# Performance work log

Measured on AMD Instinct MI355X. Metric: run time of the kernel, lower is better.

Reference implementation:

```python
import jax, jax.numpy as jnp
import numpy as np

HIDDEN = 128
IN = 28
SEQ = 28
OUT = 10
B = 16384


def _uniform(key, shape, k):
    return jax.random.uniform(key, shape, jnp.float32, -k, k)


def setup_inputs() -> dict:
    key = jax.random.key(0)
    ks = jax.random.split(key, 12)
    k = 1.0 / np.sqrt(HIDDEN)
    return {
        "x": jax.random.normal(ks[0], (B, SEQ * IN), jnp.float32),
        "w_ih_l0": _uniform(ks[1], (4 * HIDDEN, IN), k),
        "w_hh_l0": _uniform(ks[2], (4 * HIDDEN, HIDDEN), k),
        "b_ih_l0": _uniform(ks[3], (4 * HIDDEN,), k),
        "b_hh_l0": _uniform(ks[4], (4 * HIDDEN,), k),
        "w_ih_l1": _uniform(ks[5], (4 * HIDDEN, HIDDEN), k),
        "w_hh_l1": _uniform(ks[6], (4 * HIDDEN, HIDDEN), k),
        "b_ih_l1": _uniform(ks[7], (4 * HIDDEN,), k),
        "b_hh_l1": _uniform(ks[8], (4 * HIDDEN,), k),
        "fc_w": _uniform(ks[9], (OUT, HIDDEN), k),
        "fc_b": _uniform(ks[10], (OUT,), k),
    }


def _lstm_layer(x, w_ih, w_hh, b_ih, b_hh):
    # x: [B, T, D_in] -> hs: [B, T, H], hT/cT: [B, H]
    Bz = x.shape[0]
    H = w_hh.shape[1]
    # precompute input projection for all timesteps (one big GEMM)
    xp = jnp.einsum('btd,gd->btg', x, w_ih) + b_ih  # [B, T, 4H]
    xp = jnp.swapaxes(xp, 0, 1)  # [T, B, 4H]
    h0 = jnp.zeros((Bz, H), x.dtype)
    c0 = jnp.zeros((Bz, H), x.dtype)

    def step(carry, xt):
        h, c = carry
        gates = xt + h @ w_hh.T + b_hh  # [B, 4H]
        i, f, g, o = jnp.split(gates, 4, axis=-1)  # torch gate order i,f,g,o
        c_new = jax.nn.sigmoid(f) * c + jax.nn.sigmoid(i) * jnp.tanh(g)
        h_new = jax.nn.sigmoid(o) * jnp.tanh(c_new)
        return (h_new, c_new), h_new

    (hT, cT), hs = jax.lax.scan(step, (h0, c0), xp)
    return jnp.swapaxes(hs, 0, 1), hT, cT


def reference(x, w_ih_l0, w_hh_l0, b_ih_l0, b_hh_l0,
              w_ih_l1, w_hh_l1, b_ih_l1, b_hh_l1, fc_w, fc_b):
    x = x.reshape(-1, SEQ, IN)
    out0, h0T, c0T = _lstm_layer(x, w_ih_l0, w_hh_l0, b_ih_l0, b_hh_l0)
    out1, h1T, c1T = _lstm_layer(out0, w_ih_l1, w_hh_l1, b_ih_l1, b_hh_l1)
    logits = out1[:, -1, :] @ fc_w.T + fc_b  # [B, out_dim]
    h_n = jnp.stack([h0T, h1T], axis=0)  # [2, B, H]
    c_n = jnp.stack([c0T, c1T], axis=0)
    return (logits, h_n, c_n)
```

## Files before the change

kernel.cpp:

```cpp
#include <hip/hip_runtime.h>

typedef __attribute__((ext_vector_type(8))) short short8;
typedef __attribute__((ext_vector_type(4))) float f32x4;
typedef __attribute__((ext_vector_type(4))) unsigned int u32x4;

#define MFMA16(a, b, c) __builtin_amdgcn_mfma_f32_16x16x32_bf16((a), (b), (c), 0, 0, 0)

__device__ __forceinline__ unsigned short f2bf(float f) {
  unsigned int u = __builtin_bit_cast(unsigned int, f);
  u += 0x7fffu + ((u >> 16) & 1u);
  return (unsigned short)(u >> 16);
}
__device__ __forceinline__ float bf2f(unsigned short s) {
  unsigned int u = ((unsigned int)s) << 16;
  return __builtin_bit_cast(float, u);
}
__device__ __forceinline__ unsigned cvtpk(float lo, float hi) {
  unsigned r;
  asm("v_cvt_pk_bf16_f32 %0, %1, %2" : "=v"(r) : "v"(lo), "v"(hi));
  return r;
}

__device__ __forceinline__ void lstm_elem(float gi, float gf, float gg, float go,
                                          float& c, float& h) {
  const float L1 = 1.44269504f, L2 = 2.88539008f;
  float A = __builtin_amdgcn_exp2f(-L1 * gi);
  float B = __builtin_amdgcn_exp2f(L2 * gg);
  float t1 = 1.0f + B;
  float den = __builtin_amdgcn_rcpf(__builtin_fmaf(A, t1, t1));
  float it = (B - 1.0f) * den;
  float F = __builtin_amdgcn_rcpf(1.0f + __builtin_amdgcn_exp2f(-L1 * gf));
  c = __builtin_fmaf(F, c, it);
  float C = __builtin_amdgcn_exp2f(L2 * c);
  float O = __builtin_amdgcn_exp2f(-L1 * go);
  float t2 = 1.0f + C;
  float den2 = __builtin_amdgcn_rcpf(__builtin_fmaf(O, t2, t2));
  h = (C - 1.0f) * den2;
}

__global__ void prep_weights(const float* __restrict__ w_ih_l0, const float* __restrict__ w_hh_l0,
                             const float* __restrict__ w_ih_l1, const float* __restrict__ w_hh_l1,
                             unsigned short* __restrict__ W0f, unsigned short* __restrict__ W1f) {
  int tid = blockIdx.x * blockDim.x + threadIdx.x;
  if (tid < 32 * 5 * 64) {
    int nt = tid / 320, rem = tid % 320;
    int kc = rem / 64, lane = rem % 64;
    int g = nt * 16 + (lane & 15);
    int k0 = kc * 32 + (lane >> 4) * 8;
    short8 s;
#pragma unroll
    for (int j = 0; j < 8; ++j) {
      int k = k0 + j;
      float val;
      if (k < 28) val = w_ih_l0[g * 28 + k];
      else if (k < 32) val = 0.0f;
      else val = w_hh_l0[g * 128 + (k - 32)];
      s[j] = (short)f2bf(val);
    }
    *(short8*)(W0f + (size_t)tid * 8) = s;
  } else if (tid < 32 * 5 * 64 + 32 * 8 * 64) {
    int id = tid - 32 * 5 * 64;
    int nt = id / 512, rem = id % 512;
    int kc = rem / 64, lane = rem % 64;
    int g = nt * 16 + (lane & 15);
    int k0 = kc * 32 + (lane >> 4) * 8;
    short8 s;
#pragma unroll
    for (int j = 0; j < 8; ++j) {
      int k = k0 + j;
      float val = (k < 128) ? w_ih_l1[g * 128 + k] : w_hh_l1[g * 128 + (k - 128)];
      s[j] = (short)f2bf(val);
    }
    *(short8*)(W1f + (size_t)id * 8) = s;
  }
}

__global__ __launch_bounds__(512) void lstm_fused(
    const float* __restrict__ x,
    const float* __restrict__ b_ih_l0, const float* __restrict__ b_hh_l0,
    const float* __restrict__ b_ih_l1, const float* __restrict__ b_hh_l1,
    const float* __restrict__ fc_w, const float* __restrict__ fc_b,
    const unsigned short* __restrict__ W0f, const unsigned short* __restrict__ W1f,
    float* __restrict__ out) {
  __shared__ __align__(16) char hls[4 * 16384];

  const int tid = (int)threadIdx.x;
  const int wv = tid >> 6;
  const int lane = tid & 63;
  const int lr = lane & 15;
  const int lq = lane >> 4;
  const int b0 = (int)blockIdx.x * 64;

  for (int i = tid; i < 16384; i += 512) ((unsigned*)hls)[i] = 0u;

  f32x4 bias0s[4], bias1s[4];
#pragma unroll
  for (int q = 0; q < 4; ++q) {
    int g = q * 128 + wv * 16 + lr;
    float v0 = b_ih_l0[g] + b_hh_l0[g];
    float v1 = b_ih_l1[g] + b_hh_l1[g];
    f32x4 s0; s0[0] = v0; s0[1] = v0; s0[2] = v0; s0[3] = v0;
    f32x4 s1; s1[0] = v1; s1[1] = v1; s1[2] = v1; s1[3] = v1;
    bias0s[q] = s0; bias1s[q] = s1;
  }

  const unsigned rbB = (unsigned)(lr * 256 + ((lq ^ lr) << 4));
  const unsigned cwl = (unsigned)((wv * 2 + (lr >> 3)) ^ (lq << 2));
  const unsigned wbB = (unsigned)(lq * 1024 + (cwl << 4) + (lr & 7) * 2);
  const unsigned wB0 = (unsigned)((wv * 320 + lane) * 16);
  const unsigned wB1 = (unsigned)((wv * 512 + lane) * 16);
  const unsigned xo0 = (unsigned)(((b0 + lr) * 784 + lq * 8) * 4);

  float c0s[4][4], c1s[4][4];
#pragma unroll
  for (int m = 0; m < 4; ++m)
#pragma unroll
    for (int r = 0; r < 4; ++r) { c0s[m][r] = 0.0f; c1s[m][r] = 0.0f; }

  __syncthreads();

  for (int t = 0; t < 28; ++t) {
    const unsigned sp = (unsigned)(t & 1) << 14;
    const unsigned sq = sp ^ 16384u;

    f32x4 acc[4][4];

    {
      short8 ax[4];
      const char* xb = (const char*)x + (unsigned)(t * 112);
#pragma unroll
      for (int m = 0; m < 4; ++m) {
        const unsigned xo = xo0 + (unsigned)(m * 50176);
        f32x4 u0 = *(const f32x4*)(xb + xo);
        f32x4 u1 = {0.0f, 0.0f, 0.0f, 0.0f};
        if (lq < 3) u1 = *(const f32x4*)(xb + xo + 16);
        u32x4 up;
        up[0] = cvtpk(u0[0], u0[1]);
        up[1] = cvtpk(u0[2], u0[3]);
        up[2] = cvtpk(u1[0], u1[1]);
        up[3] = cvtpk(u1[2], u1[3]);
        ax[m] = __builtin_bit_cast(short8, up);
      }
      short8 bq[4];
#pragma unroll
      for (int q = 0; q < 4; ++q)
        bq[q] = *(const short8*)((const char*)W0f + (wB0 + (unsigned)(q * 40960)));
#pragma unroll
      for (int m = 0; m < 4; ++m)
#pragma unroll
        for (int q = 0; q < 4; ++q) acc[m][q] = MFMA16(ax[m], bq[q], bias0s[q]);
    }

    {
      const unsigned r0 = rbB + sq;
#pragma unroll 2
      for (int kc = 1; kc < 5; ++kc) {
        short8 bq[4];
#pragma unroll
        for (int q = 0; q < 4; ++q)
          bq[q] = *(const short8*)((const char*)W0f + (wB0 + (unsigned)(q * 40960 + kc * 1024)));
        short8 am[4];
#pragma unroll
        for (int m = 0; m < 4; ++m)
          am[m] = *(const short8*)(hls + ((r0 ^ (unsigned)((kc - 1) * 64)) + m * 4096));
#pragma unroll
        for (int m = 0; m < 4; ++m)
#pragma unroll
          for (int q = 0; q < 4; ++q) acc[m][q] = MFMA16(am[m], bq[q], acc[m][q]);
      }
    }

    {
      const unsigned wa = wbB + sp;
#pragma unroll
      for (int m = 0; m < 4; ++m) {
        float hv[4];
#pragma unroll
        for (int r = 0; r < 4; ++r) {
          float c = c0s[m][r], h;
          lstm_elem(acc[m][0][r], acc[m][1][r], acc[m][2][r], acc[m][3][r], c, h);
          c0s[m][r] = c; hv[r] = h;
        }
        unsigned u01 = cvtpk(hv[0], hv[1]);
        unsigned u23 = cvtpk(hv[2], hv[3]);
        *(unsigned short*)(hls + ((wa ^ 0u)  + m * 4096 + 0))   = (unsigned short)u01;
        *(unsigned short*)(hls + ((wa ^ 16u) + m * 4096 + 256)) = (unsigned short)(u01 >> 16);
        *(unsigned short*)(hls + ((wa ^ 32u) + m * 4096 + 512)) = (unsigned short)u23;
        *(unsigned short*)(hls + ((wa ^ 48u) + m * 4096 + 768)) = (unsigned short)(u23 >> 16);
      }
    }

    __syncthreads();

    {
      const unsigned rh0 = rbB + sp;
      const unsigned rh1 = rbB + 32768u + sq;

      {
        short8 bq[4];
#pragma unroll
        for (int q = 0; q < 4; ++q)
          bq[q] = *(const short8*)((const char*)W1f + (wB1 + (unsigned)(q * 65536)));
        short8 am[4];
#pragma unroll
        for (int m = 0; m < 4; ++m)
          am[m] = *(const short8*)(hls + (rh0 + m * 4096));
#pragma unroll
        for (int m = 0; m < 4; ++m)
#pragma unroll
          for (int q = 0; q < 4; ++q) acc[m][q] = MFMA16(am[m], bq[q], bias1s[q]);
      }
#pragma unroll 2
      for (int kc = 1; kc < 4; ++kc) {
        short8 bq[4];
#pragma unroll
        for (int q = 0; q < 4; ++q)
          bq[q] = *(const short8*)((const char*)W1f + (wB1 + (unsigned)(q * 65536 + kc * 1024)));
        short8 am[4];
#pragma unroll
        for (int m = 0; m < 4; ++m)
          am[m] = *(const short8*)(hls + ((rh0 ^ (unsigned)(kc * 64)) + m * 4096));
#pragma unroll
        for (int m = 0; m < 4; ++m)
#pragma unroll
          for (int q = 0; q < 4; ++q) acc[m][q] = MFMA16(am[m], bq[q], acc[m][q]);
      }
#pragma unroll 2
      for (int kc = 4; kc < 8; ++kc) {
        short8 bq[4];
#pragma unroll
        for (int q = 0; q < 4; ++q)
          bq[q] = *(const short8*)((const char*)W1f + (wB1 + (unsigned)(q * 65536 + kc * 1024)));
        short8 am[4];
#pragma unroll
        for (int m = 0; m < 4; ++m)
          am[m] = *(const short8*)(hls + ((rh1 ^ (unsigned)((kc - 4) * 64)) + m * 4096));
#pragma unroll
        for (int m = 0; m < 4; ++m)
#pragma unroll
          for (int q = 0; q < 4; ++q) acc[m][q] = MFMA16(am[m], bq[q], acc[m][q]);
      }
    }

    {
      const unsigned wa = wbB + 32768u + sp;
#pragma unroll
      for (int m = 0; m < 4; ++m) {
        float hv[4];
#pragma unroll
        for (int r = 0; r < 4; ++r) {
          float c = c1s[m][r], h;
          lstm_elem(acc[m][0][r], acc[m][1][r], acc[m][2][r], acc[m][3][r], c, h);
          c1s[m][r] = c; hv[r] = h;
        }
        unsigned u01 = cvtpk(hv[0], hv[1]);
        unsigned u23 = cvtpk(hv[2], hv[3]);
        *(unsigned short*)(hls + ((wa ^ 0u)  + m * 4096 + 0))   = (unsigned short)u01;
        *(unsigned short*)(hls + ((wa ^ 16u) + m * 4096 + 256)) = (unsigned short)(u01 >> 16);
        *(unsigned short*)(hls + ((wa ^ 32u) + m * 4096 + 512)) = (unsigned short)u23;
        *(unsigned short*)(hls + ((wa ^ 48u) + m * 4096 + 768)) = (unsigned short)(u23 >> 16);
      }
    }
  }

  {
    const unsigned wa0 = wbB + 16384u;
    const unsigned wa1 = wbB + 49152u;
#pragma unroll
    for (int m = 0; m < 4; ++m)
#pragma unroll
      for (int r = 0; r < 4; ++r) {
        int row = m * 16 + lq * 4 + r, col = wv * 16 + lr;
        size_t o = (size_t)(b0 + row) * 128 + col;
        unsigned roff = (unsigned)(r << 4);
        float h0 = bf2f(*(const unsigned short*)(hls + ((wa0 ^ roff) + m * 4096 + r * 256)));
        float h1 = bf2f(*(const unsigned short*)(hls + ((wa1 ^ roff) + m * 4096 + r * 256)));
        out[163840 + o] = h0;
        out[4358144 + o] = c0s[m][r];
        out[2260992 + o] = h1;
        out[6455296 + o] = c1s[m][r];
      }
  }

  __syncthreads();

  for (int it = tid; it < 640; it += 512) {
    const unsigned short* h1f = (const unsigned short*)(hls + 49152);
    int bl = it / 10, o = it % 10;
    float s = fc_b[o];
#pragma unroll
    for (int kc8 = 0; kc8 < 16; ++kc8) {
      short8 hv = *(const short8*)(h1f + bl * 128 + ((kc8 ^ (bl & 15)) << 3));
      const float* wp = fc_w + o * 128 + kc8 * 8;
#pragma unroll
      for (int j = 0; j < 8; ++j) s += bf2f((unsigned short)hv[j]) * wp[j];
    }
    out[(size_t)(b0 + bl) * 10 + o] = s;
  }
}

extern "C" void kernel_launch(void* const* d_in, const int* in_sizes, int n_in,
                              void* d_out, int out_size, void* d_ws, size_t ws_size,
                              hipStream_t stream) {
  const float* x       = (const float*)d_in[0];
  const float* w_ih_l0 = (const float*)d_in[1];
  const float* w_hh_l0 = (const float*)d_in[2];
  const float* b_ih_l0 = (const float*)d_in[3];
  const float* b_hh_l0 = (const float*)d_in[4];
  const float* w_ih_l1 = (const float*)d_in[5];
  const float* w_hh_l1 = (const float*)d_in[6];
  const float* b_ih_l1 = (const float*)d_in[7];
  const float* b_hh_l1 = (const float*)d_in[8];
  const float* fc_w    = (const float*)d_in[9];
  const float* fc_b    = (const float*)d_in[10];

  unsigned short* W0f = (unsigned short*)d_ws;
  unsigned short* W1f = W0f + 32 * 5 * 64 * 8;
  float* out = (float*)d_out;

  hipLaunchKernelGGL(prep_weights, dim3(104), dim3(256), 0, stream,
                     w_ih_l0, w_hh_l0, w_ih_l1, w_hh_l1, W0f, W1f);
  hipLaunchKernelGGL(lstm_fused, dim3(256), dim3(512), 0, stream,
                     x, b_ih_l0, b_hh_l0, b_ih_l1, b_hh_l1, fc_w, fc_b, W0f, W1f, out);
}
```

Before: 342.9 us.

## Prefetch next-step x and weight fragments, fold biases into activation exponents

Loads the next timestep's x tile and the first W0 fragment in the middle of the layer-1 activation phase, and the first W1 fragment before the layer-0 activation, so global-load latency overlaps with ALU work. Biases are no longer used as MFMA accumulator initialisers. Instead they are pre-scaled and folded into the exp2 arguments through an FMA, which frees the bias vector registers. The cost is extra live registers for the prefetched data, which may raise register pressure.

```diff
diff --git a/kernel.cpp b/kernel.cpp
--- a/kernel.cpp
+++ b/kernel.cpp
@@ -22,17 +22,18 @@
 }
 
 __device__ __forceinline__ void lstm_elem(float gi, float gf, float gg, float go,
+                                          float nbi, float nbf, float pbg, float nbo,
                                           float& c, float& h) {
   const float L1 = 1.44269504f, L2 = 2.88539008f;
-  float A = __builtin_amdgcn_exp2f(-L1 * gi);
-  float B = __builtin_amdgcn_exp2f(L2 * gg);
+  float A = __builtin_amdgcn_exp2f(__builtin_fmaf(-L1, gi, nbi));
+  float B = __builtin_amdgcn_exp2f(__builtin_fmaf(L2, gg, pbg));
   float t1 = 1.0f + B;
   float den = __builtin_amdgcn_rcpf(__builtin_fmaf(A, t1, t1));
   float it = (B - 1.0f) * den;
-  float F = __builtin_amdgcn_rcpf(1.0f + __builtin_amdgcn_exp2f(-L1 * gf));
+  float F = __builtin_amdgcn_rcpf(1.0f + __builtin_amdgcn_exp2f(__builtin_fmaf(-L1, gf, nbf)));
   c = __builtin_fmaf(F, c, it);
   float C = __builtin_amdgcn_exp2f(L2 * c);
-  float O = __builtin_amdgcn_exp2f(-L1 * go);
+  float O = __builtin_amdgcn_exp2f(__builtin_fmaf(-L1, go, nbo));
   float t2 = 1.0f + C;
   float den2 = __builtin_amdgcn_rcpf(__builtin_fmaf(O, t2, t2));
   h = (C - 1.0f) * den2;
@@ -93,16 +94,18 @@
 
   for (int i = tid; i < 16384; i += 512) ((unsigned*)hls)[i] = 0u;
 
-  f32x4 bias0s[4], bias1s[4];
+  const float L1 = 1.44269504f, L2 = 2.88539008f;
+  float nb0[4], nb1[4];
 #pragma unroll
   for (int q = 0; q < 4; ++q) {
     int g = q * 128 + wv * 16 + lr;
-    float v0 = b_ih_l0[g] + b_hh_l0[g];
-    float v1 = b_ih_l1[g] + b_hh_l1[g];
-    f32x4 s0; s0[0] = v0; s0[1] = v0; s0[2] = v0; s0[3] = v0;
-    f32x4 s1; s1[0] = v1; s1[1] = v1; s1[2] = v1; s1[3] = v1;
-    bias0s[q] = s0; bias1s[q] = s1;
-  }
+    float s0 = b_ih_l0[g] + b_hh_l0[g];
+    float s1 = b_ih_l1[g] + b_hh_l1[g];
+    float sc = (q == 2) ? L2 : -L1;
+    nb0[q] = sc * s0;
+    nb1[q] = sc * s1;
+  }
+  const f32x4 zero4 = {0.0f, 0.0f, 0.0f, 0.0f};
 
   const unsigned rbB = (unsigned)(lr * 256 + ((lq ^ lr) << 4));
   const unsigned cwl = (unsigned)((wv * 2 + (lr >> 3)) ^ (lq << 2));
@@ -117,6 +120,21 @@
 #pragma unroll
     for (int r = 0; r < 4; ++r) { c0s[m][r] = 0.0f; c1s[m][r] = 0.0f; }
 
+  f32x4 xu0[4], xu1[4];
+  short8 pw0[4];
+#pragma unroll
+  for (int m = 0; m < 4; ++m) {
+    const char* xb = (const char*)x;
+    const unsigned xo = xo0 + (unsigned)(m * 50176);
+    xu0[m] = *(const f32x4*)(xb + xo);
+    f32x4 z = {0.0f, 0.0f, 0.0f, 0.0f};
+    xu1[m] = z;
+    if (lq < 3) xu1[m] = *(const f32x4*)(xb + xo + 16);
+  }
+#pragma unroll
+  for (int q = 0; q < 4; ++q)
+    pw0[q] = *(const short8*)((const char*)W0f + (wB0 + (unsigned)(q * 40960)));
+
   __syncthreads();
 
   for (int t = 0; t < 28; ++t) {
@@ -127,28 +145,19 @@
 
     {
       short8 ax[4];
-      const char* xb = (const char*)x + (unsigned)(t * 112);
 #pragma unroll
       for (int m = 0; m < 4; ++m) {
-        const unsigned xo = xo0 + (unsigned)(m * 50176);
-        f32x4 u0 = *(const f32x4*)(xb + xo);
-        f32x4 u1 = {0.0f, 0.0f, 0.0f, 0.0f};
-        if (lq < 3) u1 = *(const f32x4*)(xb + xo + 16);
         u32x4 up;
-        up[0] = cvtpk(u0[0], u0[1]);
-        up[1] = cvtpk(u0[2], u0[3]);
-        up[2] = cvtpk(u1[0], u1[1]);
-        up[3] = cvtpk(u1[2], u1[3]);
+        up[0] = cvtpk(xu0[m][0], xu0[m][1]);
+        up[1] = cvtpk(xu0[m][2], xu0[m][3]);
+        up[2] = cvtpk(xu1[m][0], xu1[m][1]);
+        up[3] = cvtpk(xu1[m][2], xu1[m][3]);
         ax[m] = __builtin_bit_cast(short8, up);
       }
-      short8 bq[4];
-#pragma unroll
-      for (int q = 0; q < 4; ++q)
-        bq[q] = *(const short8*)((const char*)W0f + (wB0 + (unsigned)(q * 40960)));
 #pragma unroll
       for (int m = 0; m < 4; ++m)
 #pragma unroll
-        for (int q = 0; q < 4; ++q) acc[m][q] = MFMA16(ax[m], bq[q], bias0s[q]);
+        for (int q = 0; q < 4; ++q) acc[m][q] = MFMA16(ax[m], pw0[q], zero4);
     }
 
     {
@@ -170,6 +179,11 @@
       }
     }
 
+    short8 pq[4];
+#pragma unroll
+    for (int q = 0; q < 4; ++q)
+      pq[q] = *(const short8*)((const char*)W1f + (wB1 + (unsigned)(q * 65536)));
+
     {
       const unsigned wa = wbB + sp;
 #pragma unroll
@@ -178,7 +192,8 @@
 #pragma unroll
         for (int r = 0; r < 4; ++r) {
           float c = c0s[m][r], h;
-          lstm_elem(acc[m][0][r], acc[m][1][r], acc[m][2][r], acc[m][3][r], c, h);
+          lstm_elem(acc[m][0][r], acc[m][1][r], acc[m][2][r], acc[m][3][r],
+                    nb0[0], nb0[1], nb0[2], nb0[3], c, h);
           c0s[m][r] = c; hv[r] = h;
         }
         unsigned u01 = cvtpk(hv[0], hv[1]);
@@ -197,10 +212,6 @@
       const unsigned rh1 = rbB + 32768u + sq;
 
       {
-        short8 bq[4];
-#pragma unroll
-        for (int q = 0; q < 4; ++q)
-          bq[q] = *(const short8*)((const char*)W1f + (wB1 + (unsigned)(q * 65536)));
         short8 am[4];
 #pragma unroll
         for (int m = 0; m < 4; ++m)
@@ -208,7 +219,7 @@
 #pragma unroll
         for (int m = 0; m < 4; ++m)
 #pragma unroll
-          for (int q = 0; q < 4; ++q) acc[m][q] = MFMA16(am[m], bq[q], bias1s[q]);
+          for (int q = 0; q < 4; ++q) acc[m][q] = MFMA16(am[m], pq[q], zero4);
       }
 #pragma unroll 2
       for (int kc = 1; kc < 4; ++kc) {
@@ -245,12 +256,45 @@
     {
       const unsigned wa = wbB + 32768u + sp;
 #pragma unroll
-      for (int m = 0; m < 4; ++m) {
+      for (int m = 0; m < 2; ++m) {
         float hv[4];
 #pragma unroll
         for (int r = 0; r < 4; ++r) {
           float c = c1s[m][r], h;
-          lstm_elem(acc[m][0][r], acc[m][1][r], acc[m][2][r], acc[m][3][r], c, h);
+          lstm_elem(acc[m][0][r], acc[m][1][r], acc[m][2][r], acc[m][3][r],
+                    nb1[0], nb1[1], nb1[2], nb1[3], c, h);
+          c1s[m][r] = c; hv[r] = h;
+        }
+        unsigned u01 = cvtpk(hv[0], hv[1]);
+        unsigned u23 = cvtpk(hv[2], hv[3]);
+        *(unsigned short*)(hls + ((wa ^ 0u)  + m * 4096 + 0))   = (unsigned short)u01;
+        *(unsigned short*)(hls + ((wa ^ 16u) + m * 4096 + 256)) = (unsigned short)(u01 >> 16);
+        *(unsigned short*)(hls + ((wa ^ 32u) + m * 4096 + 512)) = (unsigned short)u23;
+        *(unsigned short*)(hls + ((wa ^ 48u) + m * 4096 + 768)) = (unsigned short)(u23 >> 16);
+      }
+
+      {
+        const int tn = (t < 27) ? t + 1 : 27;
+        const char* xb = (const char*)x + (unsigned)(tn * 112);
+#pragma unroll
+        for (int m = 0; m < 4; ++m) {
+          const unsigned xo = xo0 + (unsigned)(m * 50176);
+          xu0[m] = *(const f32x4*)(xb + xo);
+          if (lq < 3) xu1[m] = *(const f32x4*)(xb + xo + 16);
+        }
+#pragma unroll
+        for (int q = 0; q < 4; ++q)
+          pw0[q] = *(const short8*)((const char*)W0f + (wB0 + (unsigned)(q * 40960)));
+      }
+
+#pragma unroll
+      for (int m = 2; m < 4; ++m) {
+        float hv[4];
+#pragma unroll
+        for (int r = 0; r < 4; ++r) {
+          float c = c1s[m][r], h;
+          lstm_elem(acc[m][0][r], acc[m][1][r], acc[m][2][r], acc[m][3][r],
+                    nb1[0], nb1[1], nb1[2], nb1[3], c, h);
           c1s[m][r] = c; hv[r] = h;
         }
         unsigned u01 = cvtpk(hv[0], hv[1]);
```

Measured after the change: 336.2 us. 1.02x faster.

## Software-pipeline LSTM layers, interleaving MFMA chunks with gate math

Applied to the files above, without the earlier changes.

Restructures the time loop so layer-0 gate elementwise work for step t is interleaved with the layer-1 recurrent MFMAs on the previous layer-1 state, and layer-1 elementwise for step t is interleaved with layer-0 MFMAs for step t+1. The aim is to overlap transcendental VALU work with matrix-core work instead of running them in separate phases. Biases are folded into the exp2 arguments as pre-scaled constants rather than used as MFMA initial accumulators, so MFMAs start from zero. It adds a second accumulator set, which raises register pressure, and a second barrier per step.

```diff
diff --git a/kernel.cpp b/kernel.cpp
--- a/kernel.cpp
+++ b/kernel.cpp
@@ -22,17 +22,18 @@
 }
 
 __device__ __forceinline__ void lstm_elem(float gi, float gf, float gg, float go,
+                                          float nbi, float nbf, float pbg, float nbo,
                                           float& c, float& h) {
   const float L1 = 1.44269504f, L2 = 2.88539008f;
-  float A = __builtin_amdgcn_exp2f(-L1 * gi);
-  float B = __builtin_amdgcn_exp2f(L2 * gg);
+  float A = __builtin_amdgcn_exp2f(__builtin_fmaf(-L1, gi, nbi));
+  float B = __builtin_amdgcn_exp2f(__builtin_fmaf(L2, gg, pbg));
   float t1 = 1.0f + B;
   float den = __builtin_amdgcn_rcpf(__builtin_fmaf(A, t1, t1));
   float it = (B - 1.0f) * den;
-  float F = __builtin_amdgcn_rcpf(1.0f + __builtin_amdgcn_exp2f(-L1 * gf));
+  float F = __builtin_amdgcn_rcpf(1.0f + __builtin_amdgcn_exp2f(__builtin_fmaf(-L1, gf, nbf)));
   c = __builtin_fmaf(F, c, it);
   float C = __builtin_amdgcn_exp2f(L2 * c);
-  float O = __builtin_amdgcn_exp2f(-L1 * go);
+  float O = __builtin_amdgcn_exp2f(__builtin_fmaf(-L1, go, nbo));
   float t2 = 1.0f + C;
   float den2 = __builtin_amdgcn_rcpf(__builtin_fmaf(O, t2, t2));
   h = (C - 1.0f) * den2;
@@ -93,16 +94,18 @@
 
   for (int i = tid; i < 16384; i += 512) ((unsigned*)hls)[i] = 0u;
 
-  f32x4 bias0s[4], bias1s[4];
+  const float L1 = 1.44269504f, L2 = 2.88539008f;
+  float nb0[4], nb1[4];
 #pragma unroll
   for (int q = 0; q < 4; ++q) {
     int g = q * 128 + wv * 16 + lr;
-    float v0 = b_ih_l0[g] + b_hh_l0[g];
-    float v1 = b_ih_l1[g] + b_hh_l1[g];
-    f32x4 s0; s0[0] = v0; s0[1] = v0; s0[2] = v0; s0[3] = v0;
-    f32x4 s1; s1[0] = v1; s1[1] = v1; s1[2] = v1; s1[3] = v1;
-    bias0s[q] = s0; bias1s[q] = s1;
-  }
+    float s0 = b_ih_l0[g] + b_hh_l0[g];
+    float s1 = b_ih_l1[g] + b_hh_l1[g];
+    float sc = (q == 2) ? L2 : -L1;
+    nb0[q] = sc * s0;
+    nb1[q] = sc * s1;
+  }
+  const f32x4 zero4 = {0.0f, 0.0f, 0.0f, 0.0f};
 
   const unsigned rbB = (unsigned)(lr * 256 + ((lq ^ lr) << 4));
   const unsigned cwl = (unsigned)((wv * 2 + (lr >> 3)) ^ (lq << 2));
@@ -117,76 +120,77 @@
 #pragma unroll
     for (int r = 0; r < 4; ++r) { c0s[m][r] = 0.0f; c1s[m][r] = 0.0f; }
 
+  f32x4 acc0[4][4], acc1[4][4];
+
   __syncthreads();
+
+  {
+    short8 ax[4];
+#pragma unroll
+    for (int m = 0; m < 4; ++m) {
+      const unsigned xo = xo0 + (unsigned)(m * 50176);
+      f32x4 u0 = *(const f32x4*)((const char*)x + xo);
+      f32x4 u1 = {0.0f, 0.0f, 0.0f, 0.0f};
+      if (lq < 3) u1 = *(const f32x4*)((const char*)x + xo + 16);
+      u32x4 up;
+      up[0] = cvtpk(u0[0], u0[1]);
+      up[1] = cvtpk(u0[2], u0[3]);
+      up[2] = cvtpk(u1[0], u1[1]);
+      up[3] = cvtpk(u1[2], u1[3]);
+      ax[m] = __builtin_bit_cast(short8, up);
+    }
+    short8 bq[4];
+#pragma unroll
+    for (int q = 0; q < 4; ++q)
+      bq[q] = *(const short8*)((const char*)W0f + (wB0 + (unsigned)(q * 40960)));
+#pragma unroll
+    for (int m = 0; m < 4; ++m)
+#pragma unroll
+      for (int q = 0; q < 4; ++q) acc0[m][q] = MFMA16(ax[m], bq[q], zero4);
+  }
 
   for (int t = 0; t < 28; ++t) {
     const unsigned sp = (unsigned)(t & 1) << 14;
     const unsigned sq = sp ^ 16384u;
 
-    f32x4 acc[4][4];
-
     {
-      short8 ax[4];
-      const char* xb = (const char*)x + (unsigned)(t * 112);
-#pragma unroll
-      for (int m = 0; m < 4; ++m) {
-        const unsigned xo = xo0 + (unsigned)(m * 50176);
-        f32x4 u0 = *(const f32x4*)(xb + xo);
-        f32x4 u1 = {0.0f, 0.0f, 0.0f, 0.0f};
-        if (lq < 3) u1 = *(const f32x4*)(xb + xo + 16);
-        u32x4 up;
-        up[0] = cvtpk(u0[0], u0[1]);
-        up[1] = cvtpk(u0[2], u0[3]);
-        up[2] = cvtpk(u1[0], u1[1]);
-        up[3] = cvtpk(u1[2], u1[3]);
-        ax[m] = __builtin_bit_cast(short8, up);
-      }
-      short8 bq[4];
-#pragma unroll
-      for (int q = 0; q < 4; ++q)
-        bq[q] = *(const short8*)((const char*)W0f + (wB0 + (unsigned)(q * 40960)));
-#pragma unroll
-      for (int m = 0; m < 4; ++m)
-#pragma unroll
-        for (int q = 0; q < 4; ++q) acc[m][q] = MFMA16(ax[m], bq[q], bias0s[q]);
-    }
-
-    {
-      const unsigned r0 = rbB + sq;
-#pragma unroll 2
-      for (int kc = 1; kc < 5; ++kc) {
+      const unsigned rh1 = rbB + 32768u + sq;
+      const unsigned wa = wbB + sp;
+#pragma unroll
+      for (int j = 0; j < 4; ++j) {
         short8 bq[4];
 #pragma unroll
         for (int q = 0; q < 4; ++q)
-          bq[q] = *(const short8*)((const char*)W0f + (wB0 + (unsigned)(q * 40960 + kc * 1024)));
+          bq[q] = *(const short8*)((const char*)W1f + (wB1 + (unsigned)(q * 65536 + (4 + j) * 1024)));
         short8 am[4];
 #pragma unroll
         for (int m = 0; m < 4; ++m)
-          am[m] = *(const short8*)(hls + ((r0 ^ (unsigned)((kc - 1) * 64)) + m * 4096));
-#pragma unroll
-        for (int m = 0; m < 4; ++m)
-#pragma unroll
-          for (int q = 0; q < 4; ++q) acc[m][q] = MFMA16(am[m], bq[q], acc[m][q]);
-      }
-    }
-
-    {
-      const unsigned wa = wbB + sp;
-#pragma unroll
-      for (int m = 0; m < 4; ++m) {
+          am[m] = *(const short8*)(hls + ((rh1 ^ (unsigned)(j * 64)) + m * 4096));
+        if (j == 0) {
+#pragma unroll
+          for (int m = 0; m < 4; ++m)
+#pragma unroll
+            for (int q = 0; q < 4; ++q) acc1[m][q] = MFMA16(am[m], bq[q], zero4);
+        } else {
+#pragma unroll
+          for (int m = 0; m < 4; ++m)
+#pragma unroll
+            for (int q = 0; q < 4; ++q) acc1[m][q] = MFMA16(am[m], bq[q], acc1[m][q]);
+        }
         float hv[4];
 #pragma unroll
         for (int r = 0; r < 4; ++r) {
-          float c = c0s[m][r], h;
-          lstm_elem(acc[m][0][r], acc[m][1][r], acc[m][2][r], acc[m][3][r], c, h);
-          c0s[m][r] = c; hv[r] = h;
+          float c = c0s[j][r], h;
+          lstm_elem(acc0[j][0][r], acc0[j][1][r], acc0[j][2][r], acc0[j][3][r],
+                    nb0[0], nb0[1], nb0[2], nb0[3], c, h);
+          c0s[j][r] = c; hv[r] = h;
         }
         unsigned u01 = cvtpk(hv[0], hv[1]);
         unsigned u23 = cvtpk(hv[2], hv[3]);
-        *(unsigned short*)(hls + ((wa ^ 0u)  + m * 4096 + 0))   = (unsigned short)u01;
-        *(unsigned short*)(hls + ((wa ^ 16u) + m * 4096 + 256)) = (unsigned short)(u01 >> 16);
-        *(unsigned short*)(hls + ((wa ^ 32u) + m * 4096 + 512)) = (unsigned short)u23;
-        *(unsigned short*)(hls + ((wa ^ 48u) + m * 4096 + 768)) = (unsigned short)(u23 >> 16);
+        *(unsigned short*)(hls + ((wa ^ 0u)  + j * 4096 + 0))   = (unsigned short)u01;
+        *(unsigned short*)(hls + ((wa ^ 16u) + j * 4096 + 256)) = (unsigned short)(u01 >> 16);
+        *(unsigned short*)(hls + ((wa ^ 32u) + j * 4096 + 512)) = (unsigned short)u23;
+        *(unsigned short*)(hls + ((wa ^ 48u) + j * 4096 + 768)) = (unsigned short)(u23 >> 16);
       }
     }
 
@@ -194,24 +198,8 @@
 
     {
       const unsigned rh0 = rbB + sp;
-      const unsigned rh1 = rbB + 32768u + sq;
-
-      {
-        short8 bq[4];
-#pragma unroll
-        for (int q = 0; q < 4; ++q)
-          bq[q] = *(const short8*)((const char*)W1f + (wB1 + (unsigned)(q * 65536)));
-        short8 am[4];
-#pragma unroll
-        for (int m = 0; m < 4; ++m)
-          am[m] = *(const short8*)(hls + (rh0 + m * 4096));
-#pragma unroll
-        for (int m = 0; m < 4; ++m)
-#pragma unroll
-          for (int q = 0; q < 4; ++q) acc[m][q] = MFMA16(am[m], bq[q], bias1s[q]);
-      }
 #pragma unroll 2
-      for (int kc = 1; kc < 4; ++kc) {
+      for (int kc = 0; kc < 4; ++kc) {
         short8 bq[4];
 #pragma unroll
         for (int q = 0; q < 4; ++q)
@@ -223,44 +211,89 @@
 #pragma unroll
         for (int m = 0; m < 4; ++m)
 #pragma unroll
-          for (int q = 0; q < 4; ++q) acc[m][q] = MFMA16(am[m], bq[q], acc[m][q]);
-      }
-#pragma unroll 2
-      for (int kc = 4; kc < 8; ++kc) {
-        short8 bq[4];
-#pragma unroll
-        for (int q = 0; q < 4; ++q)
-          bq[q] = *(const short8*)((const char*)W1f + (wB1 + (unsigned)(q * 65536 + kc * 1024)));
-        short8 am[4];
-#pragma unroll
-        for (int m = 0; m < 4; ++m)
-          am[m] = *(const short8*)(hls + ((rh1 ^ (unsigned)((kc - 4) * 64)) + m * 4096));
-#pragma unroll
-        for (int m = 0; m < 4; ++m)
-#pragma unroll
-          for (int q = 0; q < 4; ++q) acc[m][q] = MFMA16(am[m], bq[q], acc[m][q]);
+          for (int q = 0; q < 4; ++q) acc1[m][q] = MFMA16(am[m], bq[q], acc1[m][q]);
       }
     }
 
     {
       const unsigned wa = wbB + 32768u + sp;
-#pragma unroll
-      for (int m = 0; m < 4; ++m) {
-        float hv[4];
-#pragma unroll
-        for (int r = 0; r < 4; ++r) {
-          float c = c1s[m][r], h;
-          lstm_elem(acc[m][0][r], acc[m][1][r], acc[m][2][r], acc[m][3][r], c, h);
-          c1s[m][r] = c; hv[r] = h;
-        }
-        unsigned u01 = cvtpk(hv[0], hv[1]);
-        unsigned u23 = cvtpk(hv[2], hv[3]);
-        *(unsigned short*)(hls + ((wa ^ 0u)  + m * 4096 + 0))   = (unsigned short)u01;
-        *(unsigned short*)(hls + ((wa ^ 16u) + m * 4096 + 256)) = (unsigned short)(u01 >> 16);
-        *(unsigned short*)(hls + ((wa ^ 32u) + m * 4096 + 512)) = (unsigned short)u23;
-        *(unsigned short*)(hls + ((wa ^ 48u) + m * 4096 + 768)) = (unsigned short)(u23 >> 16);
+      if (t < 27) {
+        const char* xb = (const char*)x + (unsigned)((t + 1) * 112);
+        short8 ax[4];
+#pragma unroll
+        for (int m = 0; m < 4; ++m) {
+          const unsigned xo = xo0 + (unsigned)(m * 50176);
+          f32x4 u0 = *(const f32x4*)(xb + xo);
+          f32x4 u1 = {0.0f, 0.0f, 0.0f, 0.0f};
+          if (lq < 3) u1 = *(const f32x4*)(xb + xo + 16);
+          u32x4 up;
+          up[0] = cvtpk(u0[0], u0[1]);
+          up[1] = cvtpk(u0[2], u0[3]);
+          up[2] = cvtpk(u1[0], u1[1]);
+          up[3] = cvtpk(u1[2], u1[3]);
+          ax[m] = __builtin_bit_cast(short8, up);
+        }
+        short8 bq0[4];
+#pragma unroll
+        for (int q = 0; q < 4; ++q)
+          bq0[q] = *(const short8*)((const char*)W0f + (wB0 + (unsigned)(q * 40960)));
+#pragma unroll
+        for (int m = 0; m < 4; ++m)
+#pragma unroll
+          for (int q = 0; q < 4; ++q) acc0[m][q] = MFMA16(ax[m], bq0[q], zero4);
+
+        const unsigned r0 = rbB + sp;
+#pragma unroll
+        for (int j = 0; j < 4; ++j) {
+          short8 bq[4];
+#pragma unroll
+          for (int q = 0; q < 4; ++q)
+            bq[q] = *(const short8*)((const char*)W0f + (wB0 + (unsigned)(q * 40960 + (1 + j) * 1024)));
+          short8 am[4];
+#pragma unroll
+          for (int m = 0; m < 4; ++m)
+            am[m] = *(const short8*)(hls + ((r0 ^ (unsigned)(j * 64)) + m * 4096));
+#pragma unroll
+          for (int m = 0; m < 4; ++m)
+#pragma unroll
+            for (int q = 0; q < 4; ++q) acc0[m][q] = MFMA16(am[m], bq[q], acc0[m][q]);
+          float hv[4];
+#pragma unroll
+          for (int r = 0; r < 4; ++r) {
+            float c = c1s[j][r], h;
+            lstm_elem(acc1[j][0][r], acc1[j][1][r], acc1[j][2][r], acc1[j][3][r],
+                      nb1[0], nb1[1], nb1[2], nb1[3], c, h);
+            c1s[j][r] = c; hv[r] = h;
+          }
+          unsigned u01 = cvtpk(hv[0], hv[1]);
+          unsigned u23 = cvtpk(hv[2], hv[3]);
+          *(unsigned short*)(hls + ((wa ^ 0u)  + j * 4096 + 0))   = (unsigned short)u01;
+          *(unsigned short*)(hls + ((wa ^ 16u) + j * 4096 + 256)) = (unsigned short)(u01 >> 16);
+          *(unsigned short*)(hls + ((wa ^ 32u) + j * 4096 + 512)) = (unsigned short)u23;
+          *(unsigned short*)(hls + ((wa ^ 48u) + j * 4096 + 768)) = (unsigned short)(u23 >> 16);
+        }
+      } else {
+#pragma unroll
+        for (int j = 0; j < 4; ++j) {
+          float hv[4];
+#pragma unroll
+          for (int r = 0; r < 4; ++r) {
+            float c = c1s[j][r], h;
+            lstm_elem(acc1[j][0][r], acc1[j][1][r], acc1[j][2][r], acc1[j][3][r],
+                      nb1[0], nb1[1], nb1[2], nb1[3], c, h);
+            c1s[j][r] = c; hv[r] = h;
+          }
+          unsigned u01 = cvtpk(hv[0], hv[1]);
+          unsigned u23 = cvtpk(hv[2], hv[3]);
+          *(unsigned short*)(hls + ((wa ^ 0u)  + j * 4096 + 0))   = (unsigned short)u01;
+          *(unsigned short*)(hls + ((wa ^ 16u) + j * 4096 + 256)) = (unsigned short)(u01 >> 16);
+          *(unsigned short*)(hls + ((wa ^ 32u) + j * 4096 + 512)) = (unsigned short)u23;
+          *(unsigned short*)(hls + ((wa ^ 48u) + j * 4096 + 768)) = (unsigned short)(u23 >> 16);
+        }
       }
     }
+
+    __syncthreads();
   }
 
   {
@@ -281,8 +314,6 @@
         out[6455296 + o] = c1s[m][r];
       }
   }
-
-  __syncthreads();
 
   for (int it = tid; it < 640; it += 512) {
     const unsigned short* h1f = (const unsigned short*)(hls + 49152);
```

Result: slower. 757.2 us (+120.8%).
